# Kernel tuning notes

Hardware: AMD Instinct MI355X
Metric: run time of the kernel (lower is better)

Reference implementation:

```python
import jax, jax.numpy as jnp
import numpy as np

N = 8192          # total genes
B = 16            # number of ragged batch groups (equal-size here: 512 each)
D = 768           # hidden_dim
NEG = -1.0e9      # mask fill value used by the original module


def setup_inputs() -> dict:
    key = jax.random.key(0)
    ks = jax.random.split(key, 10)
    s = 0.02
    inp = {
        "gene_embeddings": jax.random.normal(ks[0], (N, D), dtype=jnp.float32),
        # sorted group ids: 16 contiguous groups of 512 genes
        "batch": (jnp.arange(N) // (N // B)).astype(jnp.int64),
        "Wq": jax.random.normal(ks[1], (D, D), dtype=jnp.float32) * s,
        "bq": jnp.zeros((D,), dtype=jnp.float32),
        "Wk": jax.random.normal(ks[2], (D, D), dtype=jnp.float32) * s,
        "bk": jnp.zeros((D,), dtype=jnp.float32),
        "Wv": jax.random.normal(ks[3], (D, D), dtype=jnp.float32) * s,
        "bv": jnp.zeros((D,), dtype=jnp.float32),
        "Wo": jax.random.normal(ks[4], (D, D), dtype=jnp.float32) * s,
        "bo": jnp.zeros((D,), dtype=jnp.float32),
        "beta": jnp.ones((1,), dtype=jnp.float32) * 0.1,
    }
    return inp


def reference(gene_embeddings, batch, Wq, bq, Wk, bk, Wv, bv, Wo, bo, beta):
    # Single-head attention over full hidden_dim (num_heads unused in original).
    x = gene_embeddings
    q = x @ Wq.T + bq                      # [N, D]
    k = x @ Wk.T + bk
    v = x @ Wv.T + bv
    scale = 1.0 / jnp.sqrt(jnp.asarray(D, dtype=x.dtype))
    scores = (q @ k.T) * scale             # [N, N]
    # block-diagonal group mask + diagonal self-mask (same -1e9 fill as torch code)
    same_group = batch[:, None] == batch[None, :]
    eye = jnp.eye(N, dtype=bool)
    allow = same_group & (~eye)
    scores = jnp.where(allow, scores, NEG)
    weights = jax.nn.softmax(scores, axis=-1)   # dropout in eval mode -> identity
    dyn = weights @ v                       # [N, D]
    dyn = dyn @ Wo.T + bo
    return x + beta * dyn
```

## Files before the change

kernel.cpp:

```cpp
#include <hip/hip_runtime.h>
#include <hip/hip_bf16.h>
#include <cstdint>

using u16 = unsigned short;
using u32 = unsigned int;

typedef __bf16 bf16x8 __attribute__((ext_vector_type(8)));
typedef float  f32x4  __attribute__((ext_vector_type(4)));

__device__ __forceinline__ u32 f2b2(float a, float b) {
    __hip_bfloat162 h = __float22bfloat162_rn(float2{a, b});
    u32 u;
    __builtin_memcpy(&u, &h, 4);
    return u;
}
__device__ __forceinline__ float b2f(u16 b) {
    u32 u = (u32)b << 16;
    float f;
    __builtin_memcpy(&f, &u, 4);
    return f;
}

__device__ __forceinline__ void gload_lds16(const u16* g, u16* l) {
    __builtin_amdgcn_global_load_lds(
        (const __attribute__((address_space(1))) void*)g,
        (__attribute__((address_space(3))) void*)l,
        16, 0, 0);
}

__launch_bounds__(256)
__global__ void pack_kernel(const float* __restrict__ x,
                            const float* __restrict__ Wq,
                            const float* __restrict__ Wk,
                            const float* __restrict__ Wv,
                            const float* __restrict__ Wo,
                            const float* __restrict__ bq,
                            const float* __restrict__ bv,
                            const float* __restrict__ bo,
                            u16* __restrict__ xb,
                            u16* __restrict__ Wob,
                            u16* __restrict__ WqT,
                            u16* __restrict__ WkT,
                            u16* __restrict__ WvT,
                            float* __restrict__ czk,
                            float* __restrict__ bvoo)
{
    __shared__ u16 tl[64][72];
    const int b = blockIdx.x, tid = threadIdx.x;

    if (b < 3360) {
        int c = b * 256 + tid;
        long e = (long)c * 8;
        const float* src; u16* dst; long off;
        if (e < 6291456L) { src = x;  dst = xb;  off = e; }
        else              { src = Wo; dst = Wob; off = e - 6291456L; }
        float4 v0 = *(const float4*)(src + off);
        float4 v1 = *(const float4*)(src + off + 4);
        uint4 o;
        o.x = f2b2(v0.x, v0.y); o.y = f2b2(v0.z, v0.w);
        o.z = f2b2(v1.x, v1.y); o.w = f2b2(v1.z, v1.w);
        *(uint4*)(dst + off) = o;
    } else if (b < 3792) {
        int t = b - 3360;
        int w = t / 144, tt = t % 144;
        int tr = tt / 12, tc = tt % 12;
        const float* src0 = (w == 0) ? Wq : (w == 1) ? Wk : Wv;
        u16* dst0 = (w == 0) ? WqT : (w == 1) ? WkT : WvT;
        int lr = tid >> 2, lcb = (tid & 3) * 16;
        const float* src = src0 + (long)(tr * 64 + lr) * 768 + tc * 64 + lcb;
#pragma unroll
        for (int q = 0; q < 4; q++) {
            float4 v = *(const float4*)(src + q * 4);
            u32 p0 = f2b2(v.x, v.y), p1 = f2b2(v.z, v.w);
            tl[lr][lcb + q * 4 + 0] = (u16)p0;
            tl[lr][lcb + q * 4 + 1] = (u16)(p0 >> 16);
            tl[lr][lcb + q * 4 + 2] = (u16)p1;
            tl[lr][lcb + q * 4 + 3] = (u16)(p1 >> 16);
        }
        __syncthreads();
        int li = tid >> 2, lkb = (tid & 3) * 16;
        u16 o[16];
#pragma unroll
        for (int j = 0; j < 16; j++) o[j] = tl[lkb + j][li];
        u16* dst = dst0 + (long)(tc * 64 + li) * 768 + tr * 64 + lkb;
#pragma unroll
        for (int j = 0; j < 16; j++) dst[j] = o[j];
    } else if (b < 3984) {
        int wave = tid >> 6, lane = tid & 63;
        int j = (b - 3792) * 4 + wave;
        float acc = 0.f;
#pragma unroll
        for (int i = 0; i < 12; i++) {
            int rr = i * 64 + lane;
            acc += Wk[(long)rr * 768 + j] * bq[rr];
        }
#pragma unroll
        for (int d = 32; d; d >>= 1) acc += __shfl_xor(acc, d);
        if (lane == 0) czk[j] = acc;
    } else {
        int wave = tid >> 6, lane = tid & 63;
        int j = (b - 3984) * 4 + wave;
        float acc = 0.f;
#pragma unroll
        for (int i = 0; i < 12; i++) {
            int k = i * 64 + lane;
            acc += Wo[(long)j * 768 + k] * bv[k];
        }
#pragma unroll
        for (int d = 32; d; d >>= 1) acc += __shfl_xor(acc, d);
        if (lane == 0) bvoo[j] = acc + bo[j];
    }
}

template<int TM, int TN, int MODE>
__device__ __forceinline__ void gemm_body(
        const u16* __restrict__ A, int lda, long sAz,
        const u16* __restrict__ B, int ldb, long sBz,
        void* __restrict__ Cv, int ldc, long sCz,
        int K,
        const float* __restrict__ bias,
        float scale,
        u16* __restrict__ vTout)
{
    constexpr int FI = TM / 32;
    constexpr int FJ = TN / 32;
    constexpr int CA = TM / 64;
    constexpr int CB = TN / 64;

    __shared__ u16 As[2][TM * 32];
    __shared__ u16 Bs[2][TN * 32];

    const int tid  = threadIdx.x;
    const int g    = blockIdx.z;
    const u16* Ab = A + (long)g * sAz + (long)blockIdx.y * TM * lda;
    const u16* Bb = B + (long)g * sBz + (long)blockIdx.x * TN * ldb;

    const int wave = tid >> 6, lane = tid & 63;
    const int wm = (wave >> 1) * (TM / 2), wn = (wave & 1) * (TN / 2);
    const int ln15 = lane & 15, lq = lane >> 4;

    f32x4 acc[FI][FJ];
#pragma unroll
    for (int i = 0; i < FI; i++)
#pragma unroll
        for (int j = 0; j < FJ; j++)
            acc[i][j] = (f32x4){0.f, 0.f, 0.f, 0.f};

    const int srow = lane >> 2;
    const int sc   = ((lane & 3) ^ ((lane >> 4) & 3)) * 8;
    const u16* Ag[CA]; const u16* Bg[CB];
    int Al[CA], Bl[CB];
#pragma unroll
    for (int t = 0; t < CA; t++) {
        int c = wave * CA + t;
        Ag[t] = Ab + (long)(c * 16 + srow) * lda + sc;
        Al[t] = c * 512;
    }
#pragma unroll
    for (int t = 0; t < CB; t++) {
        int c = wave * CB + t;
        Bg[t] = Bb + (long)(c * 16 + srow) * ldb + sc;
        Bl[t] = c * 512;
    }

    const int foff = ln15 * 32 + ((lq ^ (ln15 >> 2)) * 8);
    const int nk = K >> 5;

#pragma unroll
    for (int t = 0; t < CA; t++) gload_lds16(Ag[t], &As[0][Al[t]]);
#pragma unroll
    for (int t = 0; t < CB; t++) gload_lds16(Bg[t], &Bs[0][Bl[t]]);

    for (int kt = 0; kt < nk; kt++) {
        const int cur = kt & 1;
        __syncthreads();
        if (kt + 1 < nk) {
            const int k0 = (kt + 1) * 32, nxt = cur ^ 1;
#pragma unroll
            for (int t = 0; t < CA; t++) gload_lds16(Ag[t] + k0, &As[nxt][Al[t]]);
#pragma unroll
            for (int t = 0; t < CB; t++) gload_lds16(Bg[t] + k0, &Bs[nxt][Bl[t]]);
        }

        bf16x8 af[FI], bfr[FJ];
#pragma unroll
        for (int i = 0; i < FI; i++)
            af[i] = *(const bf16x8*)&As[cur][(wm / 16 + i) * 512 + foff];
#pragma unroll
        for (int j = 0; j < FJ; j++)
            bfr[j] = *(const bf16x8*)&Bs[cur][(wn / 16 + j) * 512 + foff];
#pragma unroll
        for (int i = 0; i < FI; i++)
#pragma unroll
            for (int j = 0; j < FJ; j++)
                acc[i][j] = __builtin_amdgcn_mfma_f32_16x16x32_bf16(af[i], bfr[j], acc[i][j], 0, 0, 0);
    }

    const int baseRow = blockIdx.y * TM + wm;
    const int baseCol = blockIdx.x * TN + wn;

    if constexpr (MODE == 0) {
        if (baseCol < 768) {
            u16* C = (u16*)Cv;
#pragma unroll
            for (int i = 0; i < FI; i++)
#pragma unroll
                for (int j = 0; j < FJ; j++) {
                    int col = baseCol + j * 16 + ln15;
                    float bb = bias[col];
                    u32 p01 = f2b2(acc[i][j][0] + bb, acc[i][j][1] + bb);
                    u32 p23 = f2b2(acc[i][j][2] + bb, acc[i][j][3] + bb);
                    long r0 = (long)(baseRow + i * 16 + lq * 4) * ldc + col;
                    C[r0]           = (u16)p01;
                    C[r0 + ldc]     = (u16)(p01 >> 16);
                    C[r0 + 2 * ldc] = (u16)p23;
                    C[r0 + 3 * ldc] = (u16)(p23 >> 16);
                }
        } else {
#pragma unroll
            for (int i = 0; i < FI; i++)
#pragma unroll
                for (int j = 0; j < FJ; j++) {
                    int col = baseCol + j * 16 + ln15;
                    uint2 o;
                    o.x = f2b2(acc[i][j][0], acc[i][j][1]);
                    o.y = f2b2(acc[i][j][2], acc[i][j][3]);
                    *(uint2*)(vTout + (long)(col - 768) * 8192
                              + baseRow + i * 16 + lq * 4) = o;
                }
        }
    } else if constexpr (MODE == 5) {
        u16* C = (u16*)Cv + (long)g * sCz;
#pragma unroll
        for (int i = 0; i < FI; i++)
#pragma unroll
            for (int j = 0; j < FJ; j++) {
                int col = baseCol + j * 16 + ln15;
                float v[4];
#pragma unroll
                for (int r = 0; r < 4; r++) {
                    int row = baseRow + i * 16 + lq * 4 + r;
                    v[r] = acc[i][j][r] * scale;
                    if (row == col) v[r] = -1.0e9f;
                }
                u32 p01 = f2b2(v[0], v[1]);
                u32 p23 = f2b2(v[2], v[3]);
                long r0 = (long)(baseRow + i * 16 + lq * 4) * ldc + col;
                C[r0]           = (u16)p01;
                C[r0 + ldc]     = (u16)(p01 >> 16);
                C[r0 + 2 * ldc] = (u16)p23;
                C[r0 + 3 * ldc] = (u16)(p23 >> 16);
            }
    } else {
        u16* C = (u16*)Cv + (long)g * sCz;
#pragma unroll
        for (int i = 0; i < FI; i++)
#pragma unroll
            for (int j = 0; j < FJ; j++) {
                int col = baseCol + j * 16 + ln15;
                u32 p01 = f2b2(acc[i][j][0], acc[i][j][1]);
                u32 p23 = f2b2(acc[i][j][2], acc[i][j][3]);
                long r0 = (long)(baseRow + i * 16 + lq * 4) * ldc + col;
                C[r0]           = (u16)p01;
                C[r0 + ldc]     = (u16)(p01 >> 16);
                C[r0 + 2 * ldc] = (u16)p23;
                C[r0 + 3 * ldc] = (u16)(p23 >> 16);
            }
    }
}

__launch_bounds__(256)
__global__ void k_ww(const u16* WA, const u16* WB, void* WZplus)
{
    gemm_body<64, 128, 3>(WA, 768, 589824L, WB, 768, 589824L,
                          WZplus, 768, -589824L, 768,
                          nullptr, 0.f, nullptr);
}
__launch_bounds__(256)
__global__ void k_zv(const u16* A, const u16* B, void* C, const float* bias,
                     u16* vTout)
{
    gemm_body<128, 128, 0>(A, 768, 0, B, 768, 0, C, 768, 0, 768,
                           bias, 0.f, vTout);
}
__launch_bounds__(256)
__global__ void k_scores(const u16* A, const u16* B, void* C, float scale)
{
    gemm_body<64, 128, 5>(A, 768, 512L * 768, B, 768, 512L * 768,
                          C, 512, 512L * 512, 768,
                          nullptr, scale, nullptr);
}

__launch_bounds__(256)
__global__ void k_pvw(const u16* __restrict__ S,
                      const u16* __restrict__ vwT,
                      const u16* __restrict__ xb,
                      float* __restrict__ out,
                      const float* __restrict__ bvoo,
                      const float* __restrict__ betaPtr)
{
    __shared__ u16 Pl[32 * 512];
    __shared__ u16 Vs[2][128 * 32];

    const int ct = blockIdx.x, rt = blockIdx.y, g = blockIdx.z;
    const int tid = threadIdx.x;
    const int wave = tid >> 6, lane = tid & 63;
    const int ln15 = lane & 15, lq = lane >> 4;

    const int srow = lane >> 2;
    const int sc   = ((lane & 3) ^ ((lane >> 4) & 3)) * 8;
    const u16* Bg[2]; int Bl[2];
#pragma unroll
    for (int t = 0; t < 2; t++) {
        int c = wave * 2 + t;
        Bg[t] = vwT + (long)(ct * 128 + c * 16 + srow) * 8192 + g * 512 + sc;
        Bl[t] = c * 512;
    }
    gload_lds16(Bg[0], &Vs[0][Bl[0]]);
    gload_lds16(Bg[1], &Vs[0][Bl[1]]);

    const int r   = tid >> 3;
    const int seg = tid & 7;
    const u16* Srow = S + (long)g * 262144 + (long)(rt * 32 + r) * 512 + seg * 64;
    float e[64];
    float m = -3.0e38f;
#pragma unroll
    for (int j = 0; j < 8; j++) {
        uint4 q = *(const uint4*)(Srow + j * 8);
        u32 w[4] = {q.x, q.y, q.z, q.w};
#pragma unroll
        for (int h = 0; h < 4; h++) {
            float lo = b2f((u16)w[h]);
            float hi = b2f((u16)(w[h] >> 16));
            e[j * 8 + h * 2]     = lo;
            e[j * 8 + h * 2 + 1] = hi;
            m = fmaxf(m, fmaxf(lo, hi));
        }
    }
    m = fmaxf(m, __shfl_xor(m, 1));
    m = fmaxf(m, __shfl_xor(m, 2));
    m = fmaxf(m, __shfl_xor(m, 4));
    float sum = 0.f;
#pragma unroll
    for (int j = 0; j < 64; j++) { e[j] = __expf(e[j] - m); sum += e[j]; }
    sum += __shfl_xor(sum, 1);
    sum += __shfl_xor(sum, 2);
    sum += __shfl_xor(sum, 4);
    const float inv = 1.0f / sum;
#pragma unroll
    for (int jj = 0; jj < 8; jj++) {
        uint4 o;
        o.x = f2b2(e[jj * 8 + 0] * inv, e[jj * 8 + 1] * inv);
        o.y = f2b2(e[jj * 8 + 2] * inv, e[jj * 8 + 3] * inv);
        o.z = f2b2(e[jj * 8 + 4] * inv, e[jj * 8 + 5] * inv);
        o.w = f2b2(e[jj * 8 + 6] * inv, e[jj * 8 + 7] * inv);
        int c = seg * 8 + jj;
        *(uint4*)&Pl[(r * 64 + (c ^ (r & 7))) * 8] = o;
    }

    const int wm = (wave >> 1) * 16;
    const int wn = (wave & 1) * 64;
    const int foff = ln15 * 32 + ((lq ^ (ln15 >> 2)) * 8);
    const int prow = wm + ln15;

    f32x4 acc[4];
#pragma unroll
    for (int j = 0; j < 4; j++) acc[j] = (f32x4){0.f, 0.f, 0.f, 0.f};

    for (int kt = 0; kt < 16; kt++) {
        const int cur = kt & 1;
        __syncthreads();
        if (kt + 1 < 16) {
            const int k0 = (kt + 1) * 32, nxt = cur ^ 1;
            gload_lds16(Bg[0] + k0, &Vs[nxt][Bl[0]]);
            gload_lds16(Bg[1] + k0, &Vs[nxt][Bl[1]]);
        }
        bf16x8 ap = *(const bf16x8*)&Pl[(prow * 64 + ((kt * 4 + lq) ^ (prow & 7))) * 8];
        bf16x8 bfr[4];
#pragma unroll
        for (int j = 0; j < 4; j++)
            bfr[j] = *(const bf16x8*)&Vs[cur][(wn / 16 + j) * 512 + foff];
#pragma unroll
        for (int j = 0; j < 4; j++)
            acc[j] = __builtin_amdgcn_mfma_f32_16x16x32_bf16(ap, bfr[j], acc[j], 0, 0, 0);
    }

    const float bet = betaPtr[0];
    const long rowBase = (long)(g * 512 + rt * 32 + wm + lq * 4);
    const u16* Xr = xb + rowBase * 768;
    float* O = out + rowBase * 768;
#pragma unroll
    for (int j = 0; j < 4; j++) {
        int col = ct * 128 + wn + j * 16 + ln15;
        float bb = bvoo[col];
#pragma unroll
        for (int rr = 0; rr < 4; rr++)
            O[rr * 768 + col] = b2f(Xr[rr * 768 + col])
                                + bet * (acc[j][rr] + bb);
    }
}

extern "C" void kernel_launch(void* const* d_in, const int* in_sizes, int n_in,
                              void* d_out, int out_size, void* d_ws, size_t ws_size,
                              hipStream_t stream)
{
    const float* x    = (const float*)d_in[0];
    const float* Wq   = (const float*)d_in[2];
    const float* bq   = (const float*)d_in[3];
    const float* Wk   = (const float*)d_in[4];
    const float* bk   = (const float*)d_in[5];
    const float* Wv   = (const float*)d_in[6];
    const float* bv   = (const float*)d_in[7];
    const float* Wo   = (const float*)d_in[8];
    const float* bo   = (const float*)d_in[9];
    const float* beta = (const float*)d_in[10];
    float* out = (float*)d_out;
    (void)bk;

    char* ws = (char*)d_ws;
    u16*   zbuf = (u16*)(ws + 0);
    u16*   vwT  = (u16*)(ws + 12582912);
    u16*   xb   = (u16*)(ws + 25165824);
    u16*   S    = (u16*)(ws + 37748736);
    u16*   WA   = (u16*)(ws + 46137344);
    u16*   WB   = (u16*)(ws + 48496640);
    u16*   WZ   = (u16*)(ws + 50855936);
    float* czk  = (float*)(ws + 53215232);
    float* bvoo = (float*)(ws + 53218304);

    u16* Wob = WA;
    u16* WkT = WA + 589824;
    u16* WvT = WB;
    u16* WqT = WB + 589824;

    const float scale = 0.03608439182435161f;

    pack_kernel<<<4176, 256, 0, stream>>>(x, Wq, Wk, Wv, Wo, bq, bv, bo,
                                          xb, Wob, WqT, WkT, WvT, czk, bvoo);

    k_ww<<<dim3(6, 12, 2), 256, 0, stream>>>(WA, WB, (void*)(WZ + 589824L));

    k_zv<<<dim3(12, 64, 1), 256, 0, stream>>>(xb, WZ, (void*)zbuf, czk, vwT);

    k_scores<<<dim3(4, 8, 16), 256, 0, stream>>>(zbuf, xb, (void*)S, scale);

    k_pvw<<<dim3(6, 16, 16), 256, 0, stream>>>(S, vwT, xb, out, bvoo, beta);
}
```

Measured before the change: 208.1 us.

## Fuse scores GEMM, softmax and PV projection into one attention kernel

Replaces the separate scores kernel (which wrote a bf16 512x512 score matrix per group to global memory) and the softmax+PV kernel with one fused kernel per 32-row tile. Each block computes the scores tile into LDS, applies mask and softmax there, then loops over all six output column tiles with double-buffered vwT loads. This removes the global round trip of the score matrix and one launch. In exchange the grid shrinks to 256 blocks of 512 threads with large LDS use, so occupancy and parallelism drop, and each block redoes the P fragment work serially across column tiles.

```diff
diff --git a/kernel.cpp b/kernel.cpp
--- a/kernel.cpp
+++ b/kernel.cpp
@@ -229,28 +229,6 @@
                               + baseRow + i * 16 + lq * 4) = o;
                 }
         }
-    } else if constexpr (MODE == 5) {
-        u16* C = (u16*)Cv + (long)g * sCz;
-#pragma unroll
-        for (int i = 0; i < FI; i++)
-#pragma unroll
-            for (int j = 0; j < FJ; j++) {
-                int col = baseCol + j * 16 + ln15;
-                float v[4];
-#pragma unroll
-                for (int r = 0; r < 4; r++) {
-                    int row = baseRow + i * 16 + lq * 4 + r;
-                    v[r] = acc[i][j][r] * scale;
-                    if (row == col) v[r] = -1.0e9f;
-                }
-                u32 p01 = f2b2(v[0], v[1]);
-                u32 p23 = f2b2(v[2], v[3]);
-                long r0 = (long)(baseRow + i * 16 + lq * 4) * ldc + col;
-                C[r0]           = (u16)p01;
-                C[r0 + ldc]     = (u16)(p01 >> 16);
-                C[r0 + 2 * ldc] = (u16)p23;
-                C[r0 + 3 * ldc] = (u16)(p23 >> 16);
-            }
     } else {
         u16* C = (u16*)Cv + (long)g * sCz;
 #pragma unroll
@@ -283,120 +261,193 @@
     gemm_body<128, 128, 0>(A, 768, 0, B, 768, 0, C, 768, 0, 768,
                            bias, 0.f, vTout);
 }
-__launch_bounds__(256)
-__global__ void k_scores(const u16* A, const u16* B, void* C, float scale)
-{
-    gemm_body<64, 128, 5>(A, 768, 512L * 768, B, 768, 512L * 768,
-                          C, 512, 512L * 512, 768,
-                          nullptr, scale, nullptr);
-}
-
-__launch_bounds__(256)
-__global__ void k_pvw(const u16* __restrict__ S,
-                      const u16* __restrict__ vwT,
-                      const u16* __restrict__ xb,
-                      float* __restrict__ out,
-                      const float* __restrict__ bvoo,
-                      const float* __restrict__ betaPtr)
-{
-    __shared__ u16 Pl[32 * 512];
-    __shared__ u16 Vs[2][128 * 32];
-
-    const int ct = blockIdx.x, rt = blockIdx.y, g = blockIdx.z;
+
+__launch_bounds__(512)
+__global__ void k_fattn(const u16* __restrict__ zbuf,
+                        const u16* __restrict__ xb,
+                        const u16* __restrict__ vwT,
+                        float* __restrict__ out,
+                        const float* __restrict__ bvoo,
+                        const float* __restrict__ betaPtr,
+                        float scale)
+{
+    __shared__ __align__(16) u16 smem[57344];
+    u16* zl = smem;
+    u16* xB = smem + 24576;
+    u16* Pl = smem;
+    u16* Vs = smem + 16384;
+
+    const int rt = blockIdx.x, g = blockIdx.y;
     const int tid = threadIdx.x;
     const int wave = tid >> 6, lane = tid & 63;
     const int ln15 = lane & 15, lq = lane >> 4;
-
     const int srow = lane >> 2;
     const int sc   = ((lane & 3) ^ ((lane >> 4) & 3)) * 8;
-    const u16* Bg[2]; int Bl[2];
-#pragma unroll
-    for (int t = 0; t < 2; t++) {
-        int c = wave * 2 + t;
-        Bg[t] = vwT + (long)(ct * 128 + c * 16 + srow) * 8192 + g * 512 + sc;
+    const int foff = ln15 * 32 + ((lq ^ (ln15 >> 2)) * 8);
+
+    const long rowBase = (long)(g * 512 + rt * 32);
+    const u16* Zb = zbuf + rowBase * 768;
+    const u16* Xg = xb + (long)g * 512 * 768;
+
+    const int wm = (wave >> 2) * 16;
+    const int wn = (wave & 3) * 128;
+
+#pragma unroll
+    for (int n = 0; n < 6; n++) {
+        int cc = n * 8 + wave;
+        int zkt = cc >> 1, c = cc & 1;
+        gload_lds16(Zb + (long)(c * 16 + srow) * 768 + zkt * 32 + sc,
+                    &zl[cc * 512]);
+    }
+    const u16* Bg[4]; int Bl[4];
+#pragma unroll
+    for (int t = 0; t < 4; t++) {
+        int c = wave * 4 + t;
+        Bg[t] = Xg + (long)(c * 16 + srow) * 768 + sc;
         Bl[t] = c * 512;
     }
-    gload_lds16(Bg[0], &Vs[0][Bl[0]]);
-    gload_lds16(Bg[1], &Vs[0][Bl[1]]);
-
-    const int r   = tid >> 3;
-    const int seg = tid & 7;
-    const u16* Srow = S + (long)g * 262144 + (long)(rt * 32 + r) * 512 + seg * 64;
-    float e[64];
-    float m = -3.0e38f;
-#pragma unroll
-    for (int j = 0; j < 8; j++) {
-        uint4 q = *(const uint4*)(Srow + j * 8);
-        u32 w[4] = {q.x, q.y, q.z, q.w};
-#pragma unroll
-        for (int h = 0; h < 4; h++) {
-            float lo = b2f((u16)w[h]);
-            float hi = b2f((u16)(w[h] >> 16));
-            e[j * 8 + h * 2]     = lo;
-            e[j * 8 + h * 2 + 1] = hi;
-            m = fmaxf(m, fmaxf(lo, hi));
-        }
-    }
-    m = fmaxf(m, __shfl_xor(m, 1));
-    m = fmaxf(m, __shfl_xor(m, 2));
-    m = fmaxf(m, __shfl_xor(m, 4));
-    float sum = 0.f;
-#pragma unroll
-    for (int j = 0; j < 64; j++) { e[j] = __expf(e[j] - m); sum += e[j]; }
-    sum += __shfl_xor(sum, 1);
-    sum += __shfl_xor(sum, 2);
-    sum += __shfl_xor(sum, 4);
-    const float inv = 1.0f / sum;
-#pragma unroll
-    for (int jj = 0; jj < 8; jj++) {
-        uint4 o;
-        o.x = f2b2(e[jj * 8 + 0] * inv, e[jj * 8 + 1] * inv);
-        o.y = f2b2(e[jj * 8 + 2] * inv, e[jj * 8 + 3] * inv);
-        o.z = f2b2(e[jj * 8 + 4] * inv, e[jj * 8 + 5] * inv);
-        o.w = f2b2(e[jj * 8 + 6] * inv, e[jj * 8 + 7] * inv);
-        int c = seg * 8 + jj;
-        *(uint4*)&Pl[(r * 64 + (c ^ (r & 7))) * 8] = o;
-    }
-
-    const int wm = (wave >> 1) * 16;
-    const int wn = (wave & 1) * 64;
-    const int foff = ln15 * 32 + ((lq ^ (ln15 >> 2)) * 8);
-    const int prow = wm + ln15;
-
-    f32x4 acc[4];
-#pragma unroll
-    for (int j = 0; j < 4; j++) acc[j] = (f32x4){0.f, 0.f, 0.f, 0.f};
-
-    for (int kt = 0; kt < 16; kt++) {
+#pragma unroll
+    for (int t = 0; t < 4; t++) gload_lds16(Bg[t], &xB[Bl[t]]);
+
+    f32x4 acc[8];
+#pragma unroll
+    for (int j = 0; j < 8; j++) acc[j] = (f32x4){0.f, 0.f, 0.f, 0.f};
+
+    for (int kt = 0; kt < 24; kt++) {
         const int cur = kt & 1;
         __syncthreads();
-        if (kt + 1 < 16) {
+        if (kt + 1 < 24) {
             const int k0 = (kt + 1) * 32, nxt = cur ^ 1;
-            gload_lds16(Bg[0] + k0, &Vs[nxt][Bl[0]]);
-            gload_lds16(Bg[1] + k0, &Vs[nxt][Bl[1]]);
-        }
-        bf16x8 ap = *(const bf16x8*)&Pl[(prow * 64 + ((kt * 4 + lq) ^ (prow & 7))) * 8];
-        bf16x8 bfr[4];
-#pragma unroll
-        for (int j = 0; j < 4; j++)
-            bfr[j] = *(const bf16x8*)&Vs[cur][(wn / 16 + j) * 512 + foff];
-#pragma unroll
-        for (int j = 0; j < 4; j++)
-            acc[j] = __builtin_amdgcn_mfma_f32_16x16x32_bf16(ap, bfr[j], acc[j], 0, 0, 0);
-    }
-
+#pragma unroll
+            for (int t = 0; t < 4; t++)
+                gload_lds16(Bg[t] + k0, &xB[nxt * 16384 + Bl[t]]);
+        }
+        bf16x8 af = *(const bf16x8*)&zl[(kt * 2 + (wm >> 4)) * 512 + foff];
+        bf16x8 bfr[8];
+#pragma unroll
+        for (int j = 0; j < 8; j++)
+            bfr[j] = *(const bf16x8*)&xB[cur * 16384 + (wn / 16 + j) * 512 + foff];
+#pragma unroll
+        for (int j = 0; j < 8; j++)
+            acc[j] = __builtin_amdgcn_mfma_f32_16x16x32_bf16(af, bfr[j], acc[j], 0, 0, 0);
+    }
+
+    __syncthreads();
+
+#pragma unroll
+    for (int sub = 0; sub < 2; sub++)
+        gload_lds16(vwT + (long)(wave * 16 + srow) * 8192 + g * 512 + sub * 32 + sc,
+                    &Vs[sub * 4096 + wave * 512]);
+
+#pragma unroll
+    for (int j = 0; j < 8; j++) {
+        int col = wn + j * 16 + ln15;
+        int c8 = col >> 3, b7 = col & 7;
+#pragma unroll
+        for (int r = 0; r < 4; r++) {
+            int row = wm + lq * 4 + r;
+            float v = acc[j][r] * scale;
+            if (rt * 32 + row == col) v = -1.0e9f;
+            Pl[(row * 64 + (c8 ^ (row & 7))) * 8 + b7] = (u16)f2b2(v, v);
+        }
+    }
+    __syncthreads();
+
+    {
+        const int r = tid >> 4, seg = tid & 15;
+        float e[32];
+        float m = -3.0e38f;
+#pragma unroll
+        for (int q = 0; q < 4; q++) {
+            int c8 = seg * 4 + q;
+            uint4 qv = *(const uint4*)&Pl[(r * 64 + (c8 ^ (r & 7))) * 8];
+            u32 w[4] = {qv.x, qv.y, qv.z, qv.w};
+#pragma unroll
+            for (int h = 0; h < 4; h++) {
+                float lo = b2f((u16)w[h]);
+                float hi = b2f((u16)(w[h] >> 16));
+                e[q * 8 + h * 2]     = lo;
+                e[q * 8 + h * 2 + 1] = hi;
+                m = fmaxf(m, fmaxf(lo, hi));
+            }
+        }
+        m = fmaxf(m, __shfl_xor(m, 1));
+        m = fmaxf(m, __shfl_xor(m, 2));
+        m = fmaxf(m, __shfl_xor(m, 4));
+        m = fmaxf(m, __shfl_xor(m, 8));
+        float sum = 0.f;
+#pragma unroll
+        for (int jj = 0; jj < 32; jj++) { e[jj] = __expf(e[jj] - m); sum += e[jj]; }
+        sum += __shfl_xor(sum, 1);
+        sum += __shfl_xor(sum, 2);
+        sum += __shfl_xor(sum, 4);
+        sum += __shfl_xor(sum, 8);
+        const float inv = 1.0f / sum;
+#pragma unroll
+        for (int q = 0; q < 4; q++) {
+            int c8 = seg * 4 + q;
+            uint4 o;
+            o.x = f2b2(e[q * 8 + 0] * inv, e[q * 8 + 1] * inv);
+            o.y = f2b2(e[q * 8 + 2] * inv, e[q * 8 + 3] * inv);
+            o.z = f2b2(e[q * 8 + 4] * inv, e[q * 8 + 5] * inv);
+            o.w = f2b2(e[q * 8 + 6] * inv, e[q * 8 + 7] * inv);
+            *(uint4*)&Pl[(r * 64 + (c8 ^ (r & 7))) * 8] = o;
+        }
+    }
+    __syncthreads();
+
+    const int wnP = (wave & 3) * 32;
+    const int prow = wm + ln15;
     const float bet = betaPtr[0];
-    const long rowBase = (long)(g * 512 + rt * 32 + wm + lq * 4);
-    const u16* Xr = xb + rowBase * 768;
-    float* O = out + rowBase * 768;
-#pragma unroll
-    for (int j = 0; j < 4; j++) {
-        int col = ct * 128 + wn + j * 16 + ln15;
-        float bb = bvoo[col];
-#pragma unroll
-        for (int rr = 0; rr < 4; rr++)
-            O[rr * 768 + col] = b2f(Xr[rr * 768 + col])
-                                + bet * (acc[j][rr] + bb);
+
+    bf16x8 apr[16];
+#pragma unroll
+    for (int k4 = 0; k4 < 16; k4++)
+        apr[k4] = *(const bf16x8*)&Pl[(prow * 64 + ((k4 * 4 + lq) ^ (prow & 7))) * 8];
+
+    f32x4 accP[2];
+    accP[0] = (f32x4){0.f, 0.f, 0.f, 0.f};
+    accP[1] = (f32x4){0.f, 0.f, 0.f, 0.f};
+
+    for (int ct = 0; ct < 6; ct++) {
+#pragma unroll
+        for (int k8 = 0; k8 < 8; k8++) {
+            const int t = ct * 8 + k8;
+            const int cur = t & 1;
+            __syncthreads();
+            if (t + 1 < 48) {
+                const int tn = t + 1, ctn = tn >> 3, kn = tn & 7;
+#pragma unroll
+                for (int sub = 0; sub < 2; sub++)
+                    gload_lds16(vwT + (long)(ctn * 128 + wave * 16 + srow) * 8192
+                                    + g * 512 + kn * 64 + sub * 32 + sc,
+                                &Vs[(cur ^ 1) * 8192 + sub * 4096 + wave * 512]);
+            }
+#pragma unroll
+            for (int sub = 0; sub < 2; sub++) {
+                const int kt = k8 * 2 + sub;
+                bf16x8 b0 = *(const bf16x8*)&Vs[cur * 8192 + sub * 4096
+                                                + (wnP >> 4) * 512 + foff];
+                bf16x8 b1 = *(const bf16x8*)&Vs[cur * 8192 + sub * 4096
+                                                + ((wnP >> 4) + 1) * 512 + foff];
+                accP[0] = __builtin_amdgcn_mfma_f32_16x16x32_bf16(apr[kt], b0, accP[0], 0, 0, 0);
+                accP[1] = __builtin_amdgcn_mfma_f32_16x16x32_bf16(apr[kt], b1, accP[1], 0, 0, 0);
+            }
+        }
+        {
+            const u16* Xr = xb + (rowBase + wm + lq * 4) * 768;
+            float* O = out + (rowBase + wm + lq * 4) * 768;
+#pragma unroll
+            for (int j = 0; j < 2; j++) {
+                const int col = ct * 128 + wnP + j * 16 + ln15;
+                const float bb = bvoo[col];
+#pragma unroll
+                for (int rr = 0; rr < 4; rr++)
+                    O[rr * 768 + col] = b2f(Xr[rr * 768 + col])
+                                        + bet * (accP[j][rr] + bb);
+                accP[j] = (f32x4){0.f, 0.f, 0.f, 0.f};
+            }
+        }
     }
 }
 
@@ -421,7 +472,6 @@
     u16*   zbuf = (u16*)(ws + 0);
     u16*   vwT  = (u16*)(ws + 12582912);
     u16*   xb   = (u16*)(ws + 25165824);
-    u16*   S    = (u16*)(ws + 37748736);
     u16*   WA   = (u16*)(ws + 46137344);
     u16*   WB   = (u16*)(ws + 48496640);
     u16*   WZ   = (u16*)(ws + 50855936);
@@ -442,7 +492,6 @@
 
     k_zv<<<dim3(12, 64, 1), 256, 0, stream>>>(xb, WZ, (void*)zbuf, czk, vwT);
 
-    k_scores<<<dim3(4, 8, 16), 256, 0, stream>>>(zbuf, xb, (void*)S, scale);
-
-    k_pvw<<<dim3(6, 16, 16), 256, 0, stream>>>(S, vwT, xb, out, bvoo, beta);
-}
+    k_fattn<<<dim3(16, 16), 512, 0, stream>>>(zbuf, xb, vwT, out, bvoo, beta,
+                                              scale);
+}
```

Result: faster. 203.6 us (-2.2%).
